# Kernel tuning notes

Measured on AMD Instinct MI355X. Metric: run time of the kernel, lower is better.

## Reference

```python
import jax, jax.numpy as jnp
import numpy as np

B, C, M, N = 16, 512, 256, 4096

def setup_inputs() -> dict:
    key = jax.random.key(0)
    k1, k2, k3 = jax.random.split(key, 3)
    x = jax.random.normal(k1, (B, C, N), dtype=jnp.float32)
    # Conv1d(C, M, 1, bias=False) weight: [M, C] (kernel size 1 squeezed)
    Wk = jax.random.normal(k2, (M, C), dtype=jnp.float32) * (1.0 / np.sqrt(C))
    # Conv1d(M, C, 1, bias=False) weight: [C, M]
    Wv = jax.random.normal(k3, (C, M), dtype=jnp.float32) * (1.0 / np.sqrt(M))
    return {"x": x, "Wk": Wk, "Wv": Wv}

def reference(x, Wk, Wv):
    # attn = M_k(x): 1x1 conv == matmul over channel dim -> [B, M, N]
    attn = jnp.einsum("mc,bcn->bmn", Wk, x)
    # softmax over sequence dim N
    attn = jax.nn.softmax(attn, axis=2)
    # L1 normalization over memory-unit (channel) dim M
    attn = attn / (1e-9 + attn.sum(axis=1, keepdims=True))
    # out = M_v(attn): [B, C, N]
    out = jnp.einsum("cm,bmn->bcn", Wv, attn)
    return x + out
```

## Files before the change

kernel.cpp:

```cpp
#include <hip/hip_runtime.h>
#include <hip/hip_bf16.h>

#define Bdim 16
#define Cdim 512
#define Mdim 256
#define Ndim 4096

typedef short bf16x8 __attribute__((ext_vector_type(8)));
typedef float f32x4 __attribute__((ext_vector_type(4)));
typedef unsigned short us8 __attribute__((ext_vector_type(8)));
typedef unsigned short us4 __attribute__((ext_vector_type(4)));

__device__ __forceinline__ unsigned short f2b(float f) {
  union { float f; unsigned int u; } v; v.f = f;
  return (unsigned short)((v.u + 0x8000u) >> 16);
}
__device__ __forceinline__ float b2f(unsigned short h) {
  union { unsigned int u; float f; } v; v.u = ((unsigned int)h) << 16;
  return v.f;
}

__global__ __launch_bounds__(256) void k0_convert(
    const float* __restrict__ gWk, const float* __restrict__ gWv,
    unsigned short* __restrict__ oWk, unsigned short* __restrict__ oWv) {
  const int i = (blockIdx.x * 256 + threadIdx.x) * 4;
  f32x4 a = *reinterpret_cast<const f32x4*>(gWk + i);
  f32x4 b = *reinterpret_cast<const f32x4*>(gWv + i);
  us4 ha, hb;
#pragma unroll
  for (int j = 0; j < 4; ++j) { ha[j] = f2b(a[j]); hb[j] = f2b(b[j]); }
  *reinterpret_cast<us4*>(oWk + i) = ha;
  *reinterpret_cast<us4*>(oWv + i) = hb;
}

#define K1_XPAD 72

__global__ __launch_bounds__(256) void k1_gemm1(
    const float* __restrict__ gx, const unsigned short* __restrict__ gWkB,
    unsigned short* __restrict__ gS) {
  __shared__ unsigned short Wk_s[128 * 64];
  __shared__ unsigned short xT_s[128 * K1_XPAD];
  const int t = threadIdx.x;
  const int b = blockIdx.z;
  const int m0 = blockIdx.y * 128;
  const int n0 = blockIdx.x * 128;
  const int w = t >> 6;
  const int lane = t & 63;
  const int lr = lane & 15;
  const int lg = lane >> 4;
  const int wm = (w >> 1) * 64;
  const int wn = (w & 1) * 64;

  f32x4 acc[4][4] = {};
  const float* xb = gx + (size_t)b * Cdim * Ndim + n0;

  const int snl = t & 63;
  const int scb = (t >> 6) * 16;
  const int wrow = lane >> 3;
  const int wchk = (lane & 7) ^ (wrow & 7);

  for (int ck = 0; ck < Cdim; ck += 64) {
    {
      const unsigned short* gsrc =
          gWkB + (size_t)(m0 + w * 32 + wrow) * Cdim + ck + wchk * 8;
#pragma unroll
      for (int j = 0; j < 4; ++j) {
        __builtin_amdgcn_global_load_lds(
            (const __attribute__((address_space(1))) unsigned int*)(gsrc + (size_t)j * 8 * Cdim),
            (__attribute__((address_space(3))) unsigned int*)&Wk_s[(w * 32 + j * 8) * 64],
            16, 0, 0);
      }
    }
#pragma unroll
    for (int h = 0; h < 2; ++h) {
      const int n = snl + h * 64;
      const float* src = xb + (size_t)(ck + scb) * Ndim + n;
      float xv[16];
#pragma unroll
      for (int j = 0; j < 16; ++j) xv[j] = src[(size_t)j * Ndim];
      us8 h0, h1;
#pragma unroll
      for (int j = 0; j < 8; ++j) {
        h0[j] = (unsigned short)(__float_as_uint(xv[j]) >> 16);
        h1[j] = (unsigned short)(__float_as_uint(xv[8 + j]) >> 16);
      }
      *reinterpret_cast<us8*>(&xT_s[n * K1_XPAD + scb]) = h0;
      *reinterpret_cast<us8*>(&xT_s[n * K1_XPAD + scb + 8]) = h1;
    }
    __syncthreads();
#pragma unroll
    for (int kk = 0; kk < 64; kk += 32) {
      bf16x8 af[4], bfr[4];
#pragma unroll
      for (int mi = 0; mi < 4; ++mi) {
        const int rm = wm + mi * 16 + lr;
        af[mi] = *reinterpret_cast<const bf16x8*>(
            reinterpret_cast<const char*>(Wk_s) +
            rm * 128 + ((kk * 2 + lg * 16) ^ ((rm & 7) << 4)));
      }
#pragma unroll
      for (int ni = 0; ni < 4; ++ni)
        bfr[ni] = *reinterpret_cast<const bf16x8*>(
            &xT_s[(wn + ni * 16 + lr) * K1_XPAD + kk + lg * 8]);
#pragma unroll
      for (int mi = 0; mi < 4; ++mi)
#pragma unroll
        for (int ni = 0; ni < 4; ++ni)
          acc[mi][ni] = __builtin_amdgcn_mfma_f32_16x16x32_bf16(
              af[mi], bfr[ni], acc[mi][ni], 0, 0, 0);
    }
    __syncthreads();
  }
  unsigned short* Sb = gS + ((size_t)b * Mdim + m0 + wm) * Ndim + n0 + wn;
#pragma unroll
  for (int mi = 0; mi < 4; ++mi)
#pragma unroll
    for (int ni = 0; ni < 4; ++ni)
#pragma unroll
      for (int r = 0; r < 4; ++r) {
        int m = mi * 16 + lg * 4 + r;
        int n = ni * 16 + lr;
        Sb[(size_t)m * Ndim + n] = f2b(acc[mi][ni][r]);
      }
}

__global__ __launch_bounds__(256) void k2_rowstats(
    const unsigned short* __restrict__ gS, float2* __restrict__ stats) {
  const int m = blockIdx.x;
  const int b = blockIdx.y;
  const unsigned short* row = gS + ((size_t)b * Mdim + m) * Ndim;
  const int t = threadIdx.x;
  const int w = t >> 6;
  float v[16];
#pragma unroll
  for (int i = 0; i < 2; ++i) {
    us8 u = *reinterpret_cast<const us8*>(row + i * 2048 + t * 8);
#pragma unroll
    for (int j = 0; j < 8; ++j) v[i * 8 + j] = b2f(u[j]);
  }
  float mx = -1e30f;
#pragma unroll
  for (int i = 0; i < 16; ++i) mx = fmaxf(mx, v[i]);
#pragma unroll
  for (int o = 32; o > 0; o >>= 1) mx = fmaxf(mx, __shfl_xor(mx, o, 64));
  __shared__ float redmax[4], redsum[4];
  if ((t & 63) == 0) redmax[w] = mx;
  __syncthreads();
  mx = fmaxf(fmaxf(redmax[0], redmax[1]), fmaxf(redmax[2], redmax[3]));
  float s = 0.f;
#pragma unroll
  for (int i = 0; i < 16; ++i) s += __expf(v[i] - mx);
#pragma unroll
  for (int o = 32; o > 0; o >>= 1) s += __shfl_xor(s, o, 64);
  if ((t & 63) == 0) redsum[w] = s;
  __syncthreads();
  if (t == 0) {
    float tot = redsum[0] + redsum[1] + redsum[2] + redsum[3];
    stats[(size_t)b * Mdim + m] = make_float2(mx, 1.0f / tot);
  }
}

#define K3_PAD 264

__global__ __launch_bounds__(256) void k3_norm(
    const unsigned short* __restrict__ gS, const float2* __restrict__ stats,
    unsigned short* __restrict__ gPT) {
  __shared__ unsigned short P_s[64 * K3_PAD];
  __shared__ float cs[4][64];
  __shared__ float rtot[64];
  const int b = blockIdx.y;
  const int n0 = blockIdx.x * 64;
  const int t = threadIdx.x;
  const int w = t >> 6;
  const int l = t & 63;
  const unsigned short* Sb = gS + ((size_t)b * Mdim + w * 64) * Ndim + n0 + l;
  const float2* stb = stats + (size_t)b * Mdim + w * 64;
  float acc = 0.f;
#pragma unroll
  for (int i8 = 0; i8 < 8; ++i8) {
    us8 pk;
#pragma unroll
    for (int jj = 0; jj < 8; ++jj) {
      const int mi = i8 * 8 + jj;
      float2 st = stb[mi];
      float p = __expf(b2f(Sb[(size_t)mi * Ndim]) - st.x) * st.y;
      acc += p;
      pk[jj] = f2b(p);
    }
    *reinterpret_cast<us8*>(&P_s[l * K3_PAD + w * 64 + i8 * 8]) = pk;
  }
  cs[w][l] = acc;
  __syncthreads();
  if (w == 0) rtot[l] = 1.0f / (1e-9f + cs[0][l] + cs[1][l] + cs[2][l] + cs[3][l]);
  __syncthreads();
  const int mo = (t & 31) * 8;
#pragma unroll
  for (int j = 0; j < 8; ++j) {
    const int n = (t >> 5) + j * 8;
    const float rc = rtot[n];
    us8 pv = *reinterpret_cast<const us8*>(&P_s[n * K3_PAD + mo]);
    us8 o;
#pragma unroll
    for (int q = 0; q < 8; ++q) o[q] = f2b(b2f(pv[q]) * rc);
    *reinterpret_cast<us8*>(gPT + ((size_t)b * Ndim + n0 + n) * Mdim + mo) = o;
  }
}

#define K4_P 136

__global__ __launch_bounds__(256) void k4_gemm2(
    const float* __restrict__ gx, const unsigned short* __restrict__ gWvB,
    const unsigned short* __restrict__ gPT, float* __restrict__ gout) {
  __shared__ unsigned short Wv_s[64 * K4_P];
  __shared__ unsigned short PT_s[64 * K4_P];
  const int t = threadIdx.x;
  const int b = blockIdx.z;
  const int c0 = blockIdx.y * 64;
  const int n0 = blockIdx.x * 64;
  const int w = t >> 6;
  const int lane = t & 63;
  const int lr = lane & 15;
  const int lg = lane >> 4;
  const int wc = (w >> 1) * 32;
  const int wn = (w & 1) * 32;

  f32x4 acc[2][2] = {};

  for (int ck = 0; ck < Mdim; ck += 128) {
#pragma unroll
    for (int i = 0; i < 4; ++i) {
      int q = i * 256 + t;
      int r = q >> 4;
      int mq = (q & 15) * 8;
      us8 u = *reinterpret_cast<const us8*>(gWvB + (size_t)(c0 + r) * Mdim + ck + mq);
      *reinterpret_cast<us8*>(&Wv_s[r * K4_P + mq]) = u;
    }
#pragma unroll
    for (int i = 0; i < 4; ++i) {
      int q = i * 256 + t;
      int r = q >> 4;
      int mq = (q & 15) * 8;
      us8 u = *reinterpret_cast<const us8*>(gPT + ((size_t)b * Ndim + n0 + r) * Mdim + ck + mq);
      *reinterpret_cast<us8*>(&PT_s[r * K4_P + mq]) = u;
    }
    __syncthreads();
#pragma unroll
    for (int kk = 0; kk < 128; kk += 32) {
      bf16x8 af[2], bfr[2];
#pragma unroll
      for (int ci = 0; ci < 2; ++ci)
        af[ci] = *reinterpret_cast<const bf16x8*>(
            &Wv_s[(wc + ci * 16 + lr) * K4_P + kk + lg * 8]);
#pragma unroll
      for (int ni = 0; ni < 2; ++ni)
        bfr[ni] = *reinterpret_cast<const bf16x8*>(
            &PT_s[(wn + ni * 16 + lr) * K4_P + kk + lg * 8]);
#pragma unroll
      for (int ci = 0; ci < 2; ++ci)
#pragma unroll
        for (int ni = 0; ni < 2; ++ni)
          acc[ci][ni] = __builtin_amdgcn_mfma_f32_16x16x32_bf16(
              af[ci], bfr[ni], acc[ci][ni], 0, 0, 0);
    }
    __syncthreads();
  }
#pragma unroll
  for (int ci = 0; ci < 2; ++ci)
#pragma unroll
    for (int ni = 0; ni < 2; ++ni)
#pragma unroll
      for (int r = 0; r < 4; ++r) {
        int c = c0 + wc + ci * 16 + lg * 4 + r;
        int n = n0 + wn + ni * 16 + lr;
        size_t idx = ((size_t)b * Cdim + c) * Ndim + n;
        gout[idx] = gx[idx] + acc[ci][ni][r];
      }
}

extern "C" void kernel_launch(void* const* d_in, const int* in_sizes, int n_in,
                              void* d_out, int out_size, void* d_ws, size_t ws_size,
                              hipStream_t stream) {
  const float* x = (const float*)d_in[0];
  const float* Wk = (const float*)d_in[1];
  const float* Wv = (const float*)d_in[2];
  float* out = (float*)d_out;

  unsigned short* S = (unsigned short*)d_ws;
  unsigned short* PT = S + (size_t)Bdim * Mdim * Ndim;
  float2* stats = (float2*)(PT + (size_t)Bdim * Ndim * Mdim);
  unsigned short* WkB = (unsigned short*)(stats + Bdim * Mdim);
  unsigned short* WvB = WkB + Mdim * Cdim;

  k0_convert<<<dim3((Mdim * Cdim) / 1024), 256, 0, stream>>>(Wk, Wv, WkB, WvB);
  k1_gemm1<<<dim3(Ndim / 128, Mdim / 128, Bdim), 256, 0, stream>>>(x, WkB, S);
  k2_rowstats<<<dim3(Mdim, Bdim), 256, 0, stream>>>(S, stats);
  k3_norm<<<dim3(Ndim / 64, Bdim), 256, 0, stream>>>(S, stats, PT);
  k4_gemm2<<<dim3(Ndim / 64, Cdim / 64, Bdim), 256, 0, stream>>>(x, WvB, PT, out);
}
```

Measured before the change: 123.2 us.

## Fuse column normalization into second GEMM and apply scale in epilogue

The separate k3_norm kernel, which wrote a transposed, normalized P to workspace, is removed. Each k4 block now recomputes exp(S - max) * invsum straight from S into shared memory and accumulates the per-column sums alongside. Because the L1 normalization is linear, it is applied as a per-column scale on the GEMM result in the epilogue. This drops a kernel launch and the PT write/read round trip. In exchange, the exp work and the scalar 2-byte S loads are repeated for each of the 8 channel blocks.

```diff
diff --git a/kernel.cpp b/kernel.cpp
--- a/kernel.cpp
+++ b/kernel.cpp
@@ -160,59 +160,16 @@
   }
 }
 
-#define K3_PAD 264
-
-__global__ __launch_bounds__(256) void k3_norm(
+#define K4_P 136
+
+__global__ __launch_bounds__(256) void k4_fused(
+    const float* __restrict__ gx, const unsigned short* __restrict__ gWvB,
     const unsigned short* __restrict__ gS, const float2* __restrict__ stats,
-    unsigned short* __restrict__ gPT) {
-  __shared__ unsigned short P_s[64 * K3_PAD];
-  __shared__ float cs[4][64];
-  __shared__ float rtot[64];
-  const int b = blockIdx.y;
-  const int n0 = blockIdx.x * 64;
-  const int t = threadIdx.x;
-  const int w = t >> 6;
-  const int l = t & 63;
-  const unsigned short* Sb = gS + ((size_t)b * Mdim + w * 64) * Ndim + n0 + l;
-  const float2* stb = stats + (size_t)b * Mdim + w * 64;
-  float acc = 0.f;
-#pragma unroll
-  for (int i8 = 0; i8 < 8; ++i8) {
-    us8 pk;
-#pragma unroll
-    for (int jj = 0; jj < 8; ++jj) {
-      const int mi = i8 * 8 + jj;
-      float2 st = stb[mi];
-      float p = __expf(b2f(Sb[(size_t)mi * Ndim]) - st.x) * st.y;
-      acc += p;
-      pk[jj] = f2b(p);
-    }
-    *reinterpret_cast<us8*>(&P_s[l * K3_PAD + w * 64 + i8 * 8]) = pk;
-  }
-  cs[w][l] = acc;
-  __syncthreads();
-  if (w == 0) rtot[l] = 1.0f / (1e-9f + cs[0][l] + cs[1][l] + cs[2][l] + cs[3][l]);
-  __syncthreads();
-  const int mo = (t & 31) * 8;
-#pragma unroll
-  for (int j = 0; j < 8; ++j) {
-    const int n = (t >> 5) + j * 8;
-    const float rc = rtot[n];
-    us8 pv = *reinterpret_cast<const us8*>(&P_s[n * K3_PAD + mo]);
-    us8 o;
-#pragma unroll
-    for (int q = 0; q < 8; ++q) o[q] = f2b(b2f(pv[q]) * rc);
-    *reinterpret_cast<us8*>(gPT + ((size_t)b * Ndim + n0 + n) * Mdim + mo) = o;
-  }
-}
-
-#define K4_P 136
-
-__global__ __launch_bounds__(256) void k4_gemm2(
-    const float* __restrict__ gx, const unsigned short* __restrict__ gWvB,
-    const unsigned short* __restrict__ gPT, float* __restrict__ gout) {
+    float* __restrict__ gout) {
   __shared__ unsigned short Wv_s[64 * K4_P];
-  __shared__ unsigned short PT_s[64 * K4_P];
+  __shared__ unsigned short P_s[64 * K4_P];
+  __shared__ float cs_s[4][64];
+  __shared__ float rtot_s[64];
   const int t = threadIdx.x;
   const int b = blockIdx.z;
   const int c0 = blockIdx.y * 64;
@@ -225,6 +182,10 @@
   const int wn = (w & 1) * 32;
 
   f32x4 acc[2][2] = {};
+  float csum = 0.f;
+
+  const unsigned short* Sb = gS + (size_t)b * Mdim * Ndim + n0 + lane;
+  const float2* stb = stats + (size_t)b * Mdim;
 
   for (int ck = 0; ck < Mdim; ck += 128) {
 #pragma unroll
@@ -236,12 +197,17 @@
       *reinterpret_cast<us8*>(&Wv_s[r * K4_P + mq]) = u;
     }
 #pragma unroll
-    for (int i = 0; i < 4; ++i) {
-      int q = i * 256 + t;
-      int r = q >> 4;
-      int mq = (q & 15) * 8;
-      us8 u = *reinterpret_cast<const us8*>(gPT + ((size_t)b * Ndim + n0 + r) * Mdim + ck + mq);
-      *reinterpret_cast<us8*>(&PT_s[r * K4_P + mq]) = u;
+    for (int i8 = 0; i8 < 4; ++i8) {
+      us8 pk;
+#pragma unroll
+      for (int jj = 0; jj < 8; ++jj) {
+        const int mi = ck + w * 32 + i8 * 8 + jj;
+        const float2 st = stb[mi];
+        const float p = __expf(b2f(Sb[(size_t)mi * Ndim]) - st.x) * st.y;
+        csum += p;
+        pk[jj] = f2b(p);
+      }
+      *reinterpret_cast<us8*>(&P_s[lane * K4_P + w * 32 + i8 * 8]) = pk;
     }
     __syncthreads();
 #pragma unroll
@@ -254,7 +220,7 @@
 #pragma unroll
       for (int ni = 0; ni < 2; ++ni)
         bfr[ni] = *reinterpret_cast<const bf16x8*>(
-            &PT_s[(wn + ni * 16 + lr) * K4_P + kk + lg * 8]);
+            &P_s[(wn + ni * 16 + lr) * K4_P + kk + lg * 8]);
 #pragma unroll
       for (int ci = 0; ci < 2; ++ci)
 #pragma unroll
@@ -264,6 +230,17 @@
     }
     __syncthreads();
   }
+  cs_s[w][lane] = csum;
+  __syncthreads();
+  if (w == 0)
+    rtot_s[lane] =
+        1.0f / (1e-9f + cs_s[0][lane] + cs_s[1][lane] + cs_s[2][lane] + cs_s[3][lane]);
+  __syncthreads();
+
+  float rt[2];
+#pragma unroll
+  for (int ni = 0; ni < 2; ++ni) rt[ni] = rtot_s[wn + ni * 16 + lr];
+
 #pragma unroll
   for (int ci = 0; ci < 2; ++ci)
 #pragma unroll
@@ -273,7 +250,7 @@
         int c = c0 + wc + ci * 16 + lg * 4 + r;
         int n = n0 + wn + ni * 16 + lr;
         size_t idx = ((size_t)b * Cdim + c) * Ndim + n;
-        gout[idx] = gx[idx] + acc[ci][ni][r];
+        gout[idx] = gx[idx] + acc[ci][ni][r] * rt[ni];
       }
 }
 
@@ -286,14 +263,12 @@
   float* out = (float*)d_out;
 
   unsigned short* S = (unsigned short*)d_ws;
-  unsigned short* PT = S + (size_t)Bdim * Mdim * Ndim;
-  float2* stats = (float2*)(PT + (size_t)Bdim * Ndim * Mdim);
+  float2* stats = (float2*)(S + (size_t)Bdim * Mdim * Ndim);
   unsigned short* WkB = (unsigned short*)(stats + Bdim * Mdim);
   unsigned short* WvB = WkB + Mdim * Cdim;
 
   k0_convert<<<dim3((Mdim * Cdim) / 1024), 256, 0, stream>>>(Wk, Wv, WkB, WvB);
   k1_gemm1<<<dim3(Ndim / 128, Mdim / 128, Bdim), 256, 0, stream>>>(x, WkB, S);
   k2_rowstats<<<dim3(Mdim, Bdim), 256, 0, stream>>>(S, stats);
-  k3_norm<<<dim3(Ndim / 64, Bdim), 256, 0, stream>>>(S, stats, PT);
-  k4_gemm2<<<dim3(Ndim / 64, Cdim / 64, Bdim), 256, 0, stream>>>(x, WvB, PT, out);
-}
+  k4_fused<<<dim3(Ndim / 64, Cdim / 64, Bdim), 256, 0, stream>>>(x, WvB, S, stats, out);
+}
```

New measurement: 233.1 us. 1.89x slower.
